# Performance work log

Measured on AMD Instinct MI355X. Metric: run time of the kernel, lower is better.

Reference implementation:

```python
import jax, jax.numpy as jnp
import numpy as np

B, ROWS, COLS, D, H = 64, 7, 7, 1280, 256
S, NEG, GRU_ROWS = 5, 16, 6  # pred_steps, neg_samples, rows processed by GRU


def setup_inputs() -> dict:
    key = jax.random.key(0)
    ks = jax.random.split(key, 10)
    sc = 0.05  # keep gates/tanh out of saturation
    return {
        "encodings": jax.random.normal(ks[0], (B, ROWS, COLS, D), jnp.float32),
        "hidden": jnp.zeros((1, 1, H), jnp.float32),
        "gru_w_ih": jax.random.normal(ks[1], (3 * H, D), jnp.float32) * sc,
        "gru_w_hh": jax.random.normal(ks[2], (3 * H, H), jnp.float32) * sc,
        "gru_b_ih": jax.random.normal(ks[3], (3 * H,), jnp.float32) * sc,
        "gru_b_hh": jax.random.normal(ks[4], (3 * H,), jnp.float32) * sc,
        "wk_w": jax.random.normal(ks[5], (S, D, H), jnp.float32) * sc,
        "wk_b": jax.random.normal(ks[6], (S, D), jnp.float32) * sc,
        "neg_rows": jax.random.randint(ks[7], (B, S, GRU_ROWS, COLS, NEG), 0, ROWS, jnp.int32),
        "neg_cols": jax.random.randint(ks[8], (B, S, GRU_ROWS, COLS, NEG), 0, COLS, jnp.int32),
    }


def _gru_contexts(encodings, hidden, w_ih, w_hh, b_ih, b_hh):
    # One GRU run per (image, column) over the first 6 rows, all batched together.
    x_seq = jnp.transpose(encodings[:, :GRU_ROWS], (1, 0, 2, 3)).reshape(GRU_ROWS, B * COLS, D)
    h0 = jnp.broadcast_to(hidden.reshape(1, H), (B * COLS, H))

    def step(h, x):
        gi = x @ w_ih.T + b_ih          # [N, 3H]
        gh = h @ w_hh.T + b_hh
        i_r, i_z, i_n = jnp.split(gi, 3, axis=-1)
        h_r, h_z, h_n = jnp.split(gh, 3, axis=-1)
        r = jax.nn.sigmoid(i_r + h_r)
        z = jax.nn.sigmoid(i_z + h_z)
        n = jnp.tanh(i_n + r * h_n)
        h_new = (1.0 - z) * n + z * h
        return h_new, h_new

    _, cs = jax.lax.scan(step, h0, x_seq)              # [6, B*7, H]
    return jnp.transpose(cs.reshape(GRU_ROWS, B, COLS, H), (1, 0, 2, 3))  # [B,6,7,H]


def reference(encodings, hidden, gru_w_ih, gru_w_hh, gru_b_ih, gru_b_hh,
              wk_w, wk_b, neg_rows, neg_cols):
    contexts = _gru_contexts(encodings, hidden, gru_w_ih, gru_w_hh, gru_b_ih, gru_b_hh)

    # Predictions for every step/row/col: hardtanh(Wk[s] c + b)   [B,S,6,7,D]
    preds = jnp.clip(jnp.einsum("brch,sdh->bsrcd", contexts, wk_w)
                     + wk_b[None, :, None, None, :], -1.0, 1.0)

    # Dot of every prediction with every patch encoding of the same image.
    enc_flat = encodings.reshape(B, ROWS * COLS, D)
    dots_all = jnp.einsum("bsrcd,bqd->bsrcq", preds, enc_flat)  # [B,S,6,7,49]

    # Positive: target is encodings[img, row, col] (as in the source).
    qpos = (jnp.arange(GRU_ROWS)[:, None] * COLS + jnp.arange(COLS)[None, :])  # [6,7]
    pos = jnp.take_along_axis(dots_all, qpos[None, None, :, :, None], axis=-1)  # [B,S,6,7,1]

    # Negatives: random (row,col) patches of the same image.
    neg_q = neg_rows * COLS + neg_cols                            # [B,S,6,7,NEG]
    neg = jnp.take_along_axis(dots_all, neg_q, axis=-1)

    dots = jnp.concatenate([pos, neg], axis=-1)                   # [B,S,6,7,1+NEG]
    loss_each = -jax.nn.log_softmax(dots, axis=-1)[..., 0]
    correct = (jnp.argmax(dots, axis=-1) == 0).astype(jnp.float32)

    # Valid predictions: row in range(6 - step)
    mask = ((jnp.arange(S)[:, None] + jnp.arange(GRU_ROWS)[None, :]) < GRU_ROWS)
    mask = mask.astype(jnp.float32)[None, :, :, None]             # [1,S,6,1]
    num_preds = jnp.sum(mask) * B * COLS

    loss = jnp.sum(loss_each * mask) / num_preds
    acc = jnp.sum(correct * mask) / num_preds
    return loss, acc
```

## Files before the change

kernel.cpp:

```cpp
#include <hip/hip_runtime.h>
#include <math.h>


typedef __bf16 bf16x8 __attribute__((ext_vector_type(8)));
typedef float  f32x4  __attribute__((ext_vector_type(4)));
typedef unsigned short u16;
typedef unsigned int u32;

__device__ inline u16 f2bf(float f) {
  unsigned int u = __float_as_uint(f);
  u += 0x7fff + ((u >> 16) & 1);
  return (u16)(u >> 16);
}

__device__ inline float bf2f(u16 b) {
  u32 u = (u32)b << 16;
  return __builtin_bit_cast(float, u);
}

__device__ inline void f2bf8(const float* s, u16* o) {
  float4 v0 = *(const float4*)s, v1 = *(const float4*)(s + 4);
  o[0] = f2bf(v0.x); o[1] = f2bf(v0.y); o[2] = f2bf(v0.z); o[3] = f2bf(v0.w);
  o[4] = f2bf(v1.x); o[5] = f2bf(v1.y); o[6] = f2bf(v1.z); o[7] = f2bf(v1.w);
}

__device__ inline bf16x8 lds_frag(const char* sm, int off) {
  return __builtin_bit_cast(bf16x8, *(const uint4*)(sm + off));
}

__device__ inline void gld_lds16(const void* g, void* l) {
  __builtin_amdgcn_global_load_lds(
      (const __attribute__((address_space(1))) u32*)g,
      (__attribute__((address_space(3))) u32*)l, 16, 0, 0);
}

__device__ inline float fast_sigmoid(float x) {
  float t = __builtin_amdgcn_exp2f(-1.44269504f * x);
  return __builtin_amdgcn_rcpf(1.f + t);
}
__device__ inline float fast_tanh(float x) {
  float xc = fminf(fmaxf(x, -9.f), 9.f);
  float t = __builtin_amdgcn_exp2f(2.88539008f * xc);
  return (t - 1.f) * __builtin_amdgcn_rcpf(t + 1.f);
}
__device__ inline float fast_exp(float x) {
  return __builtin_amdgcn_exp2f(1.44269504f * x);
}
__device__ inline float fast_log(float x) {
  return __builtin_amdgcn_logf(x) * 0.69314718f;
}

#define MFMA16(a, b, c) __builtin_amdgcn_mfma_f32_16x16x32_bf16(a, b, c, 0, 0, 0)

__global__ __launch_bounds__(256) void packA(
    const float* __restrict__ enc, const float* __restrict__ w_ih,
    u16* __restrict__ enc2, u16* __restrict__ wih2, float* __restrict__ out)
{
  int tid = blockIdx.x * 256 + threadIdx.x;
  if (tid == 0) { out[0] = 0.f; out[1] = 0.f; }
  u16 o[8];
  if (tid < 430080) {
    int u = tid;
    int unit = u & 1023;
    int row = unit >> 3, sl = unit & 7;
    int tk = u >> 10;
    int k0 = tk % 20, by = tk / 20;
    int m = by * 128 + row;
    int r = m / 448, n = m - r * 448;
    int b = n / 7, c = n - b * 7;
    int slot = sl ^ (row & 7);
    f2bf8(&enc[(size_t)(b * 49 + r * 7 + c) * 1280 + k0 * 64 + slot * 8], o);
    *(uint4*)&enc2[(size_t)u * 8] = *(uint4*)o;
  } else if (tid < 552960) {
    int u = tid - 430080;
    int unit = u & 1023;
    int row = unit >> 3, sl = unit & 7;
    int tk = u >> 10;
    int k0 = tk % 20, bx = tk / 20;
    int slot = sl ^ (row & 7);
    f2bf8(&w_ih[(size_t)(bx * 128 + row) * 1280 + k0 * 64 + slot * 8], o);
    *(uint4*)&wih2[(size_t)u * 8] = *(uint4*)o;
  }
}

__global__ __launch_bounds__(256) void gi_packB(
    const u16* __restrict__ enc2, const u16* __restrict__ wih2,
    const float* __restrict__ b_ih, u16* __restrict__ gib,
    const float* __restrict__ w_hh, const float* __restrict__ wk_w,
    const float* __restrict__ enc,
    u16* __restrict__ whhpk, u16* __restrict__ wkwpk, u16* __restrict__ epk)
{
  __shared__ char sm[65536];
  const int bid = blockIdx.x;
  const int t = threadIdx.x;

  if (bid >= 126) {
    int tid = (bid - 126) * 256 + t;
    int lane = tid & 63;
    u16 o[8];
    if (tid < 655360) {
      int f = tid >> 6;
      int ks2 = f & 1, t1 = f >> 1;
      int w = t1 & 3, t2 = t1 >> 2;
      int ch = t2 % 20, b = t2 / 20;
      int q = w * 16 + (lane & 15);
      int d = ch * 64 + ks2 * 32 + (lane >> 4) * 8;
      if (q < 49) {
        f2bf8(&enc[(size_t)(b * 49 + q) * 1280 + d], o);
      } else {
#pragma unroll
        for (int j = 0; j < 8; ++j) o[j] = 0;
      }
      *(uint4*)&epk[(size_t)f * 512 + lane * 8] = *(uint4*)o;
    } else if (tid < 679936) {
      int u = tid - 655360;
      int rest = u >> 6;
      int cb = rest >> 3, ks = rest & 7;
      int w = cb / 6, nf = cb % 6;
      int g = nf >> 1, half = nf & 1;
      int col = g * 256 + w * 32 + half * 16 + (lane & 15);
      int k = ks * 32 + (lane >> 4) * 8;
      f2bf8(&w_hh[(size_t)col * 256 + k], o);
      *(uint4*)&whhpk[(size_t)u * 8] = *(uint4*)o;
    } else if (tid < 884736) {
      int u = tid - 679936;
      int f = u >> 6;
      int ks = f & 7, t1 = f >> 3;
      int w = t1 & 3, t2 = t1 >> 2;
      int ch = t2 % 20, s = t2 / 20;
      f2bf8(&wk_w[((size_t)s * 1280 + ch * 64 + w * 16 + (lane & 15)) * 256
                  + ks * 32 + (lane >> 4) * 8], o);
      *(uint4*)&wkwpk[(size_t)f * 512 + lane * 8] = *(uint4*)o;
    }
    return;
  }

  const int bx = bid % 6, by = bid / 6;
  const int lane = t & 63, w = t >> 6;
  const int wr = w >> 1, wc = w & 1;
  const int wu = t & ~63;

  f32x4 acc[4][4];
#pragma unroll
  for (int i = 0; i < 4; ++i)
#pragma unroll
    for (int j = 0; j < 4; ++j) acc[i][j] = (f32x4){0.f, 0.f, 0.f, 0.f};

  const char* ga0 = (const char*)enc2 + ((size_t)(by * 20) << 14);
  const char* gb0 = (const char*)wih2 + ((size_t)(bx * 20) << 14);

#pragma unroll
  for (int j = 0; j < 4; ++j) {
    gld_lds16(ga0 + (j * 256 + t) * 16, sm + (j * 256 + wu) * 16);
    gld_lds16(gb0 + (j * 256 + t) * 16, sm + 16384 + (j * 256 + wu) * 16);
  }

  for (int k0c = 0; k0c < 20; ++k0c) {
    char* cur = sm + (k0c & 1) * 32768;
    if (k0c + 1 < 20) {
      char* nxt = sm + ((k0c + 1) & 1) * 32768;
      const char* ga = ga0 + ((size_t)(k0c + 1) << 14);
      const char* gb = gb0 + ((size_t)(k0c + 1) << 14);
#pragma unroll
      for (int j = 0; j < 4; ++j) {
        gld_lds16(ga + (j * 256 + t) * 16, nxt + (j * 256 + wu) * 16);
        gld_lds16(gb + (j * 256 + t) * 16, nxt + 16384 + (j * 256 + wu) * 16);
      }
      asm volatile("s_waitcnt vmcnt(8)" ::: "memory");
    } else {
      asm volatile("s_waitcnt vmcnt(0)" ::: "memory");
    }
    __builtin_amdgcn_s_barrier();

#pragma unroll
    for (int ks = 0; ks < 2; ++ks) {
      bf16x8 a[4], b[4];
#pragma unroll
      for (int i = 0; i < 4; ++i) {
        int arow = wr * 64 + i * 16 + (lane & 15);
        int akb  = (ks * 64 + (lane >> 4) * 16) ^ ((arow & 7) << 4);
        a[i] = lds_frag(cur, arow * 128 + akb);
        int brow = wc * 64 + i * 16 + (lane & 15);
        int bkb  = (ks * 64 + (lane >> 4) * 16) ^ ((brow & 7) << 4);
        b[i] = lds_frag(cur + 16384, brow * 128 + bkb);
      }
#pragma unroll
      for (int i = 0; i < 4; ++i)
#pragma unroll
        for (int jn = 0; jn < 4; ++jn)
          acc[i][jn] = MFMA16(a[i], b[jn], acc[i][jn]);
    }
    __builtin_amdgcn_s_barrier();
  }

#pragma unroll
  for (int i = 0; i < 4; ++i)
#pragma unroll
    for (int jn = 0; jn < 4; ++jn) {
      int gcol = bx * 128 + wc * 64 + jn * 16 + (lane & 15);
      float bias = b_ih[gcol];
#pragma unroll
      for (int r4 = 0; r4 < 4; ++r4) {
        int grow = by * 128 + wr * 64 + i * 16 + (lane >> 4) * 4 + r4;
        gib[(size_t)grow * 768 + gcol] = f2bf(acc[i][jn][r4] + bias);
      }
    }
}

__global__ __launch_bounds__(512) void gru_fused(
    const u16* __restrict__ whh_pk, const float* __restrict__ b_hh,
    const float* __restrict__ hidden, const u16* __restrict__ gib,
    u16* __restrict__ ctxb)
{
  const int n0 = blockIdx.x * 16;
  const int t = threadIdx.x, lane = t & 63, w = t >> 6;

  __shared__ char sm[16384 + 2 * 24576];
  const int GI0 = 16384;

  const int l15 = lane & 15;
  const int seq0 = (lane >> 4) * 4;
  const int hc0 = w * 32 + l15, hc1 = w * 32 + 16 + l15;

  const float br0 = b_hh[hc0],       br1 = b_hh[hc1];
  const float bz0 = b_hh[256 + hc0], bz1 = b_hh[256 + hc1];
  const float bn0 = b_hh[512 + hc0], bn1 = b_hh[512 + hc1];

#pragma unroll
  for (int i = 0; i < 3; ++i) {
    int chunk = w * 3 + i;
    gld_lds16(gib + (size_t)n0 * 768 + chunk * 512 + lane * 8,
              sm + GI0 + chunk * 1024);
  }

  float hold[2][4];
  {
    float h0 = hidden[hc0], h1 = hidden[hc1];
#pragma unroll
    for (int r4 = 0; r4 < 4; ++r4) { hold[0][r4] = h0; hold[1][r4] = h1; }
    u16 hb0 = f2bf(h0), hb1 = f2bf(h1);
#pragma unroll
    for (int r4 = 0; r4 < 4; ++r4) {
      int seq = seq0 + r4;
      *(u16*)(sm + seq * 512 + ((hc0 * 2) ^ ((seq & 7) << 4))) = hb0;
      *(u16*)(sm + seq * 512 + ((hc1 * 2) ^ ((seq & 7) << 4))) = hb1;
    }
  }

  bf16x8 bP[3][6];
  {
    const char* pkb0 = (const char*)whh_pk + w * 49152 + lane * 16;
#pragma unroll
    for (int j = 0; j < 3; ++j)
#pragma unroll
      for (int nf = 0; nf < 6; ++nf)
        bP[j][nf] = *(const bf16x8*)(pkb0 + nf * 8192 + j * 1024);
  }
  __syncthreads();

  for (int r = 0; r < 6; ++r) {
    const char* hb  = sm + (r & 1) * 8192;
    char* hbn       = sm + ((r + 1) & 1) * 8192;
    const char* gbr = sm + GI0 + (r & 1) * 24576;

    uintptr_t pa = (uintptr_t)whh_pk;
    asm volatile("" : "+v"(pa));
    const char* pkb = (const char*)pa + w * 49152 + lane * 16;

    f32x4 acc[6];
#pragma unroll
    for (int nf = 0; nf < 6; ++nf) acc[nf] = (f32x4){0.f, 0.f, 0.f, 0.f};

#pragma unroll
    for (int ks = 0; ks < 8; ++ks) {
      const int slot = ks % 3;
      bf16x8 a = lds_frag(hb, l15 * 512 +
                          ((ks * 64 + (lane >> 4) * 16) ^ ((l15 & 7) << 4)));
#pragma unroll
      for (int nf = 0; nf < 6; ++nf) acc[nf] = MFMA16(a, bP[slot][nf], acc[nf]);
      {
        const int nk = (ks + 3) & 7;
#pragma unroll
        for (int nf = 0; nf < 6; ++nf)
          bP[slot][nf] = *(const bf16x8*)(pkb + nf * 8192 + nk * 1024);
      }
    }

    if (r + 1 < 6) {
#pragma unroll
      for (int i = 0; i < 3; ++i) {
        int chunk = w * 3 + i;
        gld_lds16(gib + (size_t)((r + 1) * 448 + n0) * 768 + chunk * 512 + lane * 8,
                  sm + GI0 + ((r + 1) & 1) * 24576 + chunk * 1024);
      }
    }

#pragma unroll
    for (int r4 = 0; r4 < 4; ++r4) {
      int seq = seq0 + r4;
      float ir0 = bf2f(*(const u16*)(gbr + (size_t)(seq * 768 + hc0) * 2));
      float iz0 = bf2f(*(const u16*)(gbr + (size_t)(seq * 768 + 256 + hc0) * 2));
      float in0 = bf2f(*(const u16*)(gbr + (size_t)(seq * 768 + 512 + hc0) * 2));
      float ir1 = bf2f(*(const u16*)(gbr + (size_t)(seq * 768 + hc1) * 2));
      float iz1 = bf2f(*(const u16*)(gbr + (size_t)(seq * 768 + 256 + hc1) * 2));
      float in1 = bf2f(*(const u16*)(gbr + (size_t)(seq * 768 + 512 + hc1) * 2));
      {
        float rg = fast_sigmoid(ir0 + acc[0][r4] + br0);
        float zg = fast_sigmoid(iz0 + acc[2][r4] + bz0);
        float ng = fast_tanh(in0 + rg * (acc[4][r4] + bn0));
        float hnew = (1.f - zg) * ng + zg * hold[0][r4];
        hold[0][r4] = hnew;
        u16 hb16 = f2bf(hnew);
        *(u16*)(hbn + seq * 512 + ((hc0 * 2) ^ ((seq & 7) << 4))) = hb16;
        ctxb[(size_t)(r * 448 + n0 + seq) * 256 + hc0] = hb16;
      }
      {
        float rg = fast_sigmoid(ir1 + acc[1][r4] + br1);
        float zg = fast_sigmoid(iz1 + acc[3][r4] + bz1);
        float ng = fast_tanh(in1 + rg * (acc[5][r4] + bn1));
        float hnew = (1.f - zg) * ng + zg * hold[1][r4];
        hold[1][r4] = hnew;
        u16 hb16 = f2bf(hnew);
        *(u16*)(hbn + seq * 512 + ((hc1 * 2) ^ ((seq & 7) << 4))) = hb16;
        ctxb[(size_t)(r * 448 + n0 + seq) * 256 + hc1] = hb16;
      }
    }
    __syncthreads();
  }
}

template<int MF>
__device__ __forceinline__ void pd_body(
    int b, int s, int Ms, int t, int lane, int w, char* sm,
    const u16* __restrict__ ctxb, const u16* __restrict__ wkwpk,
    const float* __restrict__ wk_b, const u16* __restrict__ epk,
    const int* __restrict__ neg_rows, const int* __restrict__ neg_cols,
    float* __restrict__ out)
{
  const int PT_OFF = 24576;

#pragma unroll
  for (int j = 0; j < 6; ++j) {
    int u = j * 256 + t;
    int row = u >> 5, slot = u & 31;
    int rr = row < Ms ? row : 0;
    int r = rr / 7, c = rr - r * 7;
    uint4 v = *(const uint4*)&ctxb[((size_t)(r * 448 + b * 7 + c)) * 256 + slot * 8];
    int off = row * 512 + ((slot * 16) ^ ((row & 7) << 4));
    *(uint4*)(sm + off) = v;
  }
  __syncthreads();

  bf16x8 a1[MF][8];
#pragma unroll
  for (int m = 0; m < MF; ++m)
#pragma unroll
    for (int ks = 0; ks < 8; ++ks) {
      int row = m * 16 + (lane & 15);
      int kb  = (ks * 64 + (lane >> 4) * 16) ^ ((row & 7) << 4);
      a1[m][ks] = lds_frag(sm, row * 512 + kb);
    }

  f32x4 acc2[MF];
#pragma unroll
  for (int m = 0; m < MF; ++m) acc2[m] = (f32x4){0.f, 0.f, 0.f, 0.f};

  const char* wfB = (const char*)wkwpk + ((size_t)(s * 20) * 4 + w) * 8192 + lane * 16;
  const char* efB = (const char*)epk   + ((size_t)(b * 20) * 4 + w) * 2048 + lane * 16;
  const int colL = w * 16 + (lane & 15);

  bf16x8 wF[8];
#pragma unroll
  for (int ks = 0; ks < 8; ++ks)
    wF[ks] = *(const bf16x8*)(wfB + ks * 1024);

  for (int ch = 0; ch < 20; ++ch) {
    char* pt = sm + PT_OFF + (ch & 1) * 6144;

    f32x4 acc1[MF];
#pragma unroll
    for (int m = 0; m < MF; ++m) acc1[m] = (f32x4){0.f, 0.f, 0.f, 0.f};
#pragma unroll
    for (int ks = 0; ks < 8; ++ks) {
#pragma unroll
      for (int m = 0; m < MF; ++m) acc1[m] = MFMA16(a1[m][ks], wF[ks], acc1[m]);
    }
    if (ch + 1 < 20) {
      const char* wfn = wfB + (size_t)(ch + 1) * 4 * 8192;
#pragma unroll
      for (int ks = 0; ks < 8; ++ks)
        wF[ks] = *(const bf16x8*)(wfn + ks * 1024);
    }
    {
      float bias = wk_b[s * 1280 + ch * 64 + colL];
#pragma unroll
      for (int m = 0; m < MF; ++m)
#pragma unroll
        for (int r4 = 0; r4 < 4; ++r4) {
          float p = acc1[m][r4] + bias;
          p = fminf(fmaxf(p, -1.f), 1.f);
          int prow = m * 16 + (lane >> 4) * 4 + r4;
          *(u16*)(pt + prow * 128 + ((colL * 2) ^ ((prow & 7) << 4))) = f2bf(p);
        }
    }
    const char* ef = efB + (size_t)ch * 4 * 2048;
    bf16x8 e0 = *(const bf16x8*)ef;
    bf16x8 e1 = *(const bf16x8*)(ef + 1024);
    __syncthreads();

#pragma unroll
    for (int m = 0; m < MF; ++m) {
      int prow = m * 16 + (lane & 15);
      bf16x8 pf0 = lds_frag(pt, prow * 128 +
                            (((lane >> 4) * 16) ^ ((prow & 7) << 4)));
      acc2[m] = MFMA16(pf0, e0, acc2[m]);
      bf16x8 pf1 = lds_frag(pt, prow * 128 +
                            ((64 + (lane >> 4) * 16) ^ ((prow & 7) << 4)));
      acc2[m] = MFMA16(pf1, e1, acc2[m]);
    }
  }

  float* dtile = (float*)sm;
#pragma unroll
  for (int m = 0; m < MF; ++m)
#pragma unroll
    for (int r4 = 0; r4 < 4; ++r4) {
      int row = m * 16 + (lane >> 4) * 4 + r4;
      int q = w * 16 + (lane & 15);
      dtile[row * 65 + q] = acc2[m][r4];
    }
  __syncthreads();

  if (w == 0) {
    float lsum = 0.f, csum = 0.f;
    if (lane < Ms) {
      int rr = lane;
      int r = rr / 7, c = rr - r * 7;
      const float* drow = &dtile[rr * 65];
      float d0 = drow[rr];
      const int nbase = (((b * 5 + s) * 6 + r) * 7 + c) * 16;
      float mx = d0;
      float d[16];
#pragma unroll
      for (int j = 0; j < 16; ++j) {
        int q = neg_rows[nbase + j] * 7 + neg_cols[nbase + j];
        d[j] = drow[q];
        mx = fmaxf(mx, d[j]);
      }
      float se = fast_exp(d0 - mx);
#pragma unroll
      for (int j = 0; j < 16; ++j) se += fast_exp(d[j] - mx);
      lsum = -(d0 - mx - fast_log(se));
      csum = (d0 >= mx) ? 1.f : 0.f;
    }
#pragma unroll
    for (int off = 32; off > 0; off >>= 1) {
      lsum += __shfl_down(lsum, off);
      csum += __shfl_down(csum, off);
    }
    if (lane == 0) {
      atomicAdd(&out[0], lsum * (1.f / 8960.f));
      atomicAdd(&out[1], csum * (1.f / 8960.f));
    }
  }
}

__global__ __launch_bounds__(256) void fused_pd(
    const u16* __restrict__ ctxb, const u16* __restrict__ wkwpk,
    const float* __restrict__ wk_b, const u16* __restrict__ epk,
    const int* __restrict__ neg_rows, const int* __restrict__ neg_cols,
    float* __restrict__ out)
{
  const int b = blockIdx.x;
  const int s = blockIdx.y;
  const int Ms = (6 - s) * 7;
  const int t = threadIdx.x;
  const int lane = t & 63, w = t >> 6;

  __shared__ uint4 smem4[36864 / 16];
  char* sm = (char*)smem4;

  if (s < 2)      pd_body<3>(b, s, Ms, t, lane, w, sm, ctxb, wkwpk, wk_b, epk,
                             neg_rows, neg_cols, out);
  else if (s < 4) pd_body<2>(b, s, Ms, t, lane, w, sm, ctxb, wkwpk, wk_b, epk,
                             neg_rows, neg_cols, out);
  else            pd_body<1>(b, s, Ms, t, lane, w, sm, ctxb, wkwpk, wk_b, epk,
                             neg_rows, neg_cols, out);
}

extern "C" void kernel_launch(void* const* d_in, const int* in_sizes, int n_in,
                              void* d_out, int out_size, void* d_ws, size_t ws_size,
                              hipStream_t stream)
{
  const float* enc    = (const float*)d_in[0];
  const float* hidden = (const float*)d_in[1];
  const float* w_ih   = (const float*)d_in[2];
  const float* w_hh   = (const float*)d_in[3];
  const float* b_ih   = (const float*)d_in[4];
  const float* b_hh   = (const float*)d_in[5];
  const float* wk_w   = (const float*)d_in[6];
  const float* wk_b   = (const float*)d_in[7];
  const int* neg_rows = (const int*)d_in[8];
  const int* neg_cols = (const int*)d_in[9];
  float* out = (float*)d_out;

  u16*   gib   = (u16*)d_ws;
  u16*   ctxb  = gib + 6 * 448 * 768;
  u16*   whhpk = ctxb + 6 * 448 * 256;
  u16*   wkwpk = whhpk + 24576 * 8;
  u16*   epk   = wkwpk + 204800 * 8;
  u16*   enc2  = epk + 655360 * 8;
  u16*   wih2  = enc2 + 430080 * 8;

  packA<<<2160, 256, 0, stream>>>(enc, w_ih, enc2, wih2, out);

  gi_packB<<<3582, 256, 0, stream>>>(enc2, wih2, b_ih, gib,
                                     w_hh, wk_w, enc, whhpk, wkwpk, epk);

  gru_fused<<<28, 512, 0, stream>>>(whhpk, b_hh, hidden, gib, ctxb);

  fused_pd<<<dim3(64, 5), 256, 0, stream>>>(ctxb, wkwpk, wk_b, epk,
                                            neg_rows, neg_cols, out);
}
```

Measured before the change: 87.07 us.

## Move encoding and Wk packing into GRU kernel to overlap with recurrence

The bf16 packing of the encodings and Wk weights moves out of the gi_packB kernel and into extra blocks of the GRU kernel. The 28 GRU blocks are latency-bound, so these packing blocks can run on otherwise idle compute units while the recurrence proceeds. gi_packB keeps only the W_hh packing, which the GRU blocks need before they start. The risk is that packing blocks get scheduled ahead of or alongside the GRU blocks and compete with them for bandwidth.

```diff
diff --git a/kernel.cpp b/kernel.cpp
--- a/kernel.cpp
+++ b/kernel.cpp
@@ -86,9 +86,7 @@
 __global__ __launch_bounds__(256) void gi_packB(
     const u16* __restrict__ enc2, const u16* __restrict__ wih2,
     const float* __restrict__ b_ih, u16* __restrict__ gib,
-    const float* __restrict__ w_hh, const float* __restrict__ wk_w,
-    const float* __restrict__ enc,
-    u16* __restrict__ whhpk, u16* __restrict__ wkwpk, u16* __restrict__ epk)
+    const float* __restrict__ w_hh, u16* __restrict__ whhpk)
 {
   __shared__ char sm[65536];
   const int bid = blockIdx.x;
@@ -98,40 +96,14 @@
     int tid = (bid - 126) * 256 + t;
     int lane = tid & 63;
     u16 o[8];
-    if (tid < 655360) {
-      int f = tid >> 6;
-      int ks2 = f & 1, t1 = f >> 1;
-      int w = t1 & 3, t2 = t1 >> 2;
-      int ch = t2 % 20, b = t2 / 20;
-      int q = w * 16 + (lane & 15);
-      int d = ch * 64 + ks2 * 32 + (lane >> 4) * 8;
-      if (q < 49) {
-        f2bf8(&enc[(size_t)(b * 49 + q) * 1280 + d], o);
-      } else {
-#pragma unroll
-        for (int j = 0; j < 8; ++j) o[j] = 0;
-      }
-      *(uint4*)&epk[(size_t)f * 512 + lane * 8] = *(uint4*)o;
-    } else if (tid < 679936) {
-      int u = tid - 655360;
-      int rest = u >> 6;
-      int cb = rest >> 3, ks = rest & 7;
-      int w = cb / 6, nf = cb % 6;
-      int g = nf >> 1, half = nf & 1;
-      int col = g * 256 + w * 32 + half * 16 + (lane & 15);
-      int k = ks * 32 + (lane >> 4) * 8;
-      f2bf8(&w_hh[(size_t)col * 256 + k], o);
-      *(uint4*)&whhpk[(size_t)u * 8] = *(uint4*)o;
-    } else if (tid < 884736) {
-      int u = tid - 679936;
-      int f = u >> 6;
-      int ks = f & 7, t1 = f >> 3;
-      int w = t1 & 3, t2 = t1 >> 2;
-      int ch = t2 % 20, s = t2 / 20;
-      f2bf8(&wk_w[((size_t)s * 1280 + ch * 64 + w * 16 + (lane & 15)) * 256
-                  + ks * 32 + (lane >> 4) * 8], o);
-      *(uint4*)&wkwpk[(size_t)f * 512 + lane * 8] = *(uint4*)o;
-    }
+    int rest = tid >> 6;
+    int cb = rest >> 3, ks = rest & 7;
+    int w = cb / 6, nf = cb % 6;
+    int g = nf >> 1, half = nf & 1;
+    int col = g * 256 + w * 32 + half * 16 + (lane & 15);
+    int k = ks * 32 + (lane >> 4) * 8;
+    f2bf8(&w_hh[(size_t)col * 256 + k], o);
+    *(uint4*)&whhpk[(size_t)tid * 8] = *(uint4*)o;
     return;
   }
 
@@ -207,16 +179,50 @@
     }
 }
 
-__global__ __launch_bounds__(512) void gru_fused(
+__global__ __launch_bounds__(512) void gru_packC(
     const u16* __restrict__ whh_pk, const float* __restrict__ b_hh,
     const float* __restrict__ hidden, const u16* __restrict__ gib,
-    u16* __restrict__ ctxb)
+    u16* __restrict__ ctxb,
+    const float* __restrict__ enc, const float* __restrict__ wk_w,
+    u16* __restrict__ epk, u16* __restrict__ wkwpk)
 {
-  const int n0 = blockIdx.x * 16;
+  const int bid = blockIdx.x;
   const int t = threadIdx.x, lane = t & 63, w = t >> 6;
+
+  if (bid >= 28) {
+    int tid = (bid - 28) * 512 + t;
+    int ln = tid & 63;
+    u16 o[8];
+    if (tid < 655360) {
+      int f = tid >> 6;
+      int ks2 = f & 1, t1 = f >> 1;
+      int ww = t1 & 3, t2 = t1 >> 2;
+      int ch = t2 % 20, b = t2 / 20;
+      int q = ww * 16 + (ln & 15);
+      int d = ch * 64 + ks2 * 32 + (ln >> 4) * 8;
+      if (q < 49) {
+        f2bf8(&enc[(size_t)(b * 49 + q) * 1280 + d], o);
+      } else {
+#pragma unroll
+        for (int j = 0; j < 8; ++j) o[j] = 0;
+      }
+      *(uint4*)&epk[(size_t)f * 512 + ln * 8] = *(uint4*)o;
+    } else if (tid < 860160) {
+      int u = tid - 655360;
+      int f = u >> 6;
+      int ks = f & 7, t1 = f >> 3;
+      int ww = t1 & 3, t2 = t1 >> 2;
+      int ch = t2 % 20, s = t2 / 20;
+      f2bf8(&wk_w[((size_t)s * 1280 + ch * 64 + ww * 16 + (ln & 15)) * 256
+                  + ks * 32 + (ln >> 4) * 8], o);
+      *(uint4*)&wkwpk[(size_t)f * 512 + ln * 8] = *(uint4*)o;
+    }
+    return;
+  }
 
   __shared__ char sm[16384 + 2 * 24576];
   const int GI0 = 16384;
+  const int n0 = bid * 16;
 
   const int l15 = lane & 15;
   const int seq0 = (lane >> 4) * 4;
@@ -514,10 +520,10 @@
 
   packA<<<2160, 256, 0, stream>>>(enc, w_ih, enc2, wih2, out);
 
-  gi_packB<<<3582, 256, 0, stream>>>(enc2, wih2, b_ih, gib,
-                                     w_hh, wk_w, enc, whhpk, wkwpk, epk);
-
-  gru_fused<<<28, 512, 0, stream>>>(whhpk, b_hh, hidden, gib, ctxb);
+  gi_packB<<<222, 256, 0, stream>>>(enc2, wih2, b_ih, gib, w_hh, whhpk);
+
+  gru_packC<<<1708, 512, 0, stream>>>(whhpk, b_hh, hidden, gib, ctxb,
+                                      enc, wk_w, epk, wkwpk);
 
   fused_pd<<<dim3(64, 5), 256, 0, stream>>>(ctxb, wkwpk, wk_b, epk,
                                             neg_rows, neg_cols, out);
```

New measurement: 88.28 us. About the same (+1.4%).
